# Performance work log

Hardware: AMD Instinct MI355X
Metric: run time of the kernel (lower is better)

The kernel has to match this reference:

```python
import jax, jax.numpy as jnp
import numpy as np

N_EMBD = 1024
N_HEAD = 16
B, T = 2, 2048


def setup_inputs() -> dict:
    key = jax.random.key(0)
    ks = jax.random.split(key, 9)
    s = 1.0 / np.sqrt(N_EMBD)
    return {
        "x": jax.random.normal(ks[0], (B, T, N_EMBD), dtype=jnp.float32),
        "Wq": jax.random.normal(ks[1], (N_EMBD, N_EMBD), dtype=jnp.float32) * s,
        "bq": jax.random.normal(ks[2], (N_EMBD,), dtype=jnp.float32) * s,
        "Wk": jax.random.normal(ks[3], (N_EMBD, N_EMBD), dtype=jnp.float32) * s,
        "bk": jax.random.normal(ks[4], (N_EMBD,), dtype=jnp.float32) * s,
        "Wv": jax.random.normal(ks[5], (N_EMBD, N_EMBD), dtype=jnp.float32) * s,
        "bv": jax.random.normal(ks[6], (N_EMBD,), dtype=jnp.float32) * s,
        "Wp": jax.random.normal(ks[7], (N_EMBD, N_EMBD), dtype=jnp.float32) * s,
        "bp": jax.random.normal(ks[8], (N_EMBD,), dtype=jnp.float32) * s,
    }


def reference(x, Wq, bq, Wk, bk, Wv, bv, Wp, bp):
    b, t, c = x.shape
    hd = c // N_HEAD  # head dim
    # torch Linear: x @ W.T + b; reshape to (B, H, T, hd)
    def heads(W, bias):
        return (x @ W.T + bias).reshape(b, t, N_HEAD, hd).transpose(0, 2, 1, 3)
    q, k, v = heads(Wq, bq), heads(Wk, bk), heads(Wv, bv)
    scale = 1.0 / np.sqrt(hd)
    att = jnp.einsum("bhqd,bhkd->bhqk", q, k) * scale  # (B,H,T,T)
    causal = jnp.tril(jnp.ones((t, t), dtype=bool))
    att = jnp.where(causal[None, None], att, -jnp.inf)
    att = jax.nn.softmax(att, axis=-1)
    y = jnp.einsum("bhqk,bhkd->bhqd", att, v)
    y = y.transpose(0, 2, 1, 3).reshape(b, t, c)
    return y @ Wp.T + bp
```

## Files before the change

### kernel.cpp

```cpp
#include <hip/hip_runtime.h>

typedef __bf16 bf16x8 __attribute__((ext_vector_type(8)));
typedef __bf16 bf16x4 __attribute__((ext_vector_type(4)));
typedef float f32x4 __attribute__((ext_vector_type(4)));

#define DEVI __device__ __forceinline__

constexpr int NE = 1024;
constexpr int NH = 16;
constexpr int HD = 64;
constexpr int BB = 2;
constexpr int TT = 2048;
constexpr int MM = BB * TT;

DEVI unsigned short f2bf(float f) {
  union { float f; unsigned u; } v; v.f = f;
  unsigned r = v.u + 0x7FFFu + ((v.u >> 16) & 1u);
  return (unsigned short)(r >> 16);
}

__global__ __launch_bounds__(256) void cvt_bf16(const float* __restrict__ in,
                                                unsigned short* __restrict__ out, int n4) {
  int i = blockIdx.x * blockDim.x + threadIdx.x;
  if (i >= n4) return;
  float4 v = reinterpret_cast<const float4*>(in)[i];
  ushort4 o;
  o.x = f2bf(v.x); o.y = f2bf(v.y); o.z = f2bf(v.z); o.w = f2bf(v.w);
  reinterpret_cast<ushort4*>(out)[i] = o;
}

__global__ __launch_bounds__(256) void cvt_w(const float* __restrict__ q, const float* __restrict__ k,
                                             const float* __restrict__ v, const float* __restrict__ p,
                                             unsigned short* __restrict__ out) {
  int i = blockIdx.x * blockDim.x + threadIdx.x;
  const int seg = i >> 18;
  const float* src = (seg == 0) ? q : (seg == 1) ? k : (seg == 2) ? v : p;
  float4 vv = reinterpret_cast<const float4*>(src)[i & 0x3FFFF];
  ushort4 o;
  o.x = f2bf(vv.x); o.y = f2bf(vv.y); o.z = f2bf(vv.z); o.w = f2bf(vv.w);
  reinterpret_cast<ushort4*>(out)[i] = o;
}

template <int BM, int MODE>
__global__ __launch_bounds__(256, (BM == 128) ? 3 : 2)
void gemm_nt(const unsigned short* __restrict__ A, const unsigned short* __restrict__ Bm,
             const float* __restrict__ b0, const float* __restrict__ b1, const float* __restrict__ b2,
             void* __restrict__ o0, unsigned short* __restrict__ o1, unsigned short* __restrict__ o2,
             int K, int nbx) {
  constexpr int WAVES_N = (BM == 128) ? 2 : 4;
  constexpr int NJ = (BM == 128) ? 4 : 2;
  constexpr int A_LPW = BM / 64;
  __shared__ __align__(16) unsigned short As[3][BM * 32];
  __shared__ __align__(16) unsigned short Bs[3][128 * 32];
  const int tid = threadIdx.x;
  const int wid = tid >> 6;
  const int lane = tid & 63;
  const int l15 = lane & 15, l4 = lane >> 4;

  const int id = blockIdx.x;
  const int chunk = gridDim.x >> 3;
  const int idp = (id & 7) * chunk + (id >> 3);
  const int bx = idp / (gridDim.x / nbx), by = idp % (gridDim.x / nbx);

  const int brow = by * BM;
  const int bcol = bx * 128;
  const int wm = wid / WAVES_N, wn = wid % WAVES_N;
  const int wmoff = wm * 64;
  const int wnoff = wn * (128 / WAVES_N);

  f32x4 acc[4][NJ] = {};

  const int srow = lane >> 2;
  const int sscol = ((lane & 3) ^ ((lane >> 3) & 3)) * 8;

  auto stage = [&](int buf, int t) {
    const int kb = t * 32;
#pragma unroll
    for (int c = 0; c < A_LPW; ++c) {
      const int rb = wid * (BM / 4) + c * 16;
      __builtin_amdgcn_global_load_lds(
          (const __attribute__((address_space(1))) void*)(A + (size_t)(brow + rb + srow) * K + kb + sscol),
          (__attribute__((address_space(3))) void*)&As[buf][rb * 32], 16, 0, 0);
    }
#pragma unroll
    for (int c = 0; c < 2; ++c) {
      const int rb = wid * 32 + c * 16;
      __builtin_amdgcn_global_load_lds(
          (const __attribute__((address_space(1))) void*)(Bm + (size_t)(bcol + rb + srow) * K + kb + sscol),
          (__attribute__((address_space(3))) void*)&Bs[buf][rb * 32], 16, 0, 0);
    }
  };

  const int roff = l15 * 32 + (l4 ^ ((l15 >> 1) & 3)) * 8;

  auto compute = [&](int cb) {
    bf16x8 af[4], bfj[NJ];
#pragma unroll
    for (int i = 0; i < 4; ++i)
      af[i] = *reinterpret_cast<const bf16x8*>(&As[cb][(wmoff + i * 16) * 32 + roff]);
#pragma unroll
    for (int j = 0; j < NJ; ++j)
      bfj[j] = *reinterpret_cast<const bf16x8*>(&Bs[cb][(wnoff + j * 16) * 32 + roff]);
#pragma unroll
    for (int i = 0; i < 4; ++i)
#pragma unroll
      for (int j = 0; j < NJ; ++j)
        acc[i][j] = __builtin_amdgcn_mfma_f32_16x16x32_bf16(af[i], bfj[j], acc[i][j], 0, 0, 0);
  };

  const int NT = K / 32;
  stage(0, 0);
  stage(1, 1);
  int cb = 0, sb = 2;
  for (int t = 0; t + 2 < NT; ++t) {
    stage(sb, t + 2);
    if constexpr (BM == 128) asm volatile("s_waitcnt vmcnt(8)" ::: "memory");
    else                     asm volatile("s_waitcnt vmcnt(6)" ::: "memory");
    asm volatile("s_barrier" ::: "memory");
    compute(cb);
    asm volatile("s_barrier" ::: "memory");
    sb = cb;
    cb = (cb == 2) ? 0 : cb + 1;
  }
  if constexpr (BM == 128) asm volatile("s_waitcnt vmcnt(4)" ::: "memory");
  else                     asm volatile("s_waitcnt vmcnt(3)" ::: "memory");
  asm volatile("s_barrier" ::: "memory");
  compute(cb);
  asm volatile("s_barrier" ::: "memory");
  cb = (cb == 2) ? 0 : cb + 1;
  asm volatile("s_waitcnt vmcnt(0)" ::: "memory");
  asm volatile("s_barrier" ::: "memory");
  compute(cb);

  if (MODE == 0) {
#pragma unroll
    for (int j = 0; j < NJ; ++j) {
      const int col = bcol + wnoff + j * 16 + l15;
      const float bv = b0[col];
#pragma unroll
      for (int i = 0; i < 4; ++i) {
        const int row0 = brow + wmoff + i * 16 + l4 * 4;
#pragma unroll
        for (int r = 0; r < 4; ++r)
          ((float*)o0)[(size_t)(row0 + r) * NE + col] = acc[i][j][r] + bv;
      }
    }
  } else {
    const int seg = bcol >> 10;
    const float* bsel = (seg == 0) ? b0 : (seg == 1) ? b1 : b2;
    unsigned short* qk = (seg == 0) ? (unsigned short*)o0 : o1;
#pragma unroll
    for (int j = 0; j < NJ; ++j) {
      const int col = bcol + wnoff + j * 16 + l15;
      const int dcol = col & 1023;
      const int h = dcol >> 6, d = dcol & 63;
      const float bv = bsel[dcol];
#pragma unroll
      for (int i = 0; i < 4; ++i) {
        const int row0 = brow + wmoff + i * 16 + l4 * 4;
#pragma unroll
        for (int r = 0; r < 4; ++r) {
          const int row = row0 + r;
          const int b = row >> 11, t = row & (TT - 1);
          const unsigned short val = f2bf(acc[i][j][r] + bv);
          if (seg < 2)
            qk[((size_t)((b * NH + h) * TT + t) << 6) + d] = val;
          else
            o2[((size_t)(b * NH + h) * HD + d) * TT + t] = val;
        }
      }
    }
  }
}

__global__ __launch_bounds__(256, 2)
void attn(const unsigned short* __restrict__ Q, const unsigned short* __restrict__ Kk,
          const unsigned short* __restrict__ Vt, unsigned short* __restrict__ Y) {
  __shared__ __align__(16) unsigned short Ks[2][128 * 64];
  __shared__ __align__(16) unsigned short Vs[2][64 * 128];
  __shared__ __align__(16) unsigned short Pw[4][32 * 64];
  const int tid = threadIdx.x, wid = tid >> 6, lane = tid & 63;
  const int l15 = lane & 15, l4 = lane >> 4;

  const int id = blockIdx.x;
  const int j = id & 255, kk = id >> 8;
  const int bh = (j & 15) + 16 * kk;
  const int xt = kk ? 15 - (j >> 4) : (j >> 4);

  const int qw = xt * 128 + wid * 32;
  const int nkb = xt + 1;
  const unsigned short* Qh = Q + (size_t)bh * TT * HD;
  const unsigned short* Kh = Kk + (size_t)bh * TT * HD;
  const unsigned short* Vh = Vt + (size_t)bh * HD * TT;

  bf16x8 qf[2][2];
#pragma unroll
  for (int qt = 0; qt < 2; ++qt)
#pragma unroll
    for (int ks = 0; ks < 2; ++ks) {
      bf16x8 t = *reinterpret_cast<const bf16x8*>(&Qh[(qw + qt * 16 + l15) * 64 + ks * 32 + l4 * 8]);
#pragma unroll
      for (int e = 0; e < 8; ++e) t[e] = (__bf16)((float)t[e] * 0.18033688011f);
      qf[qt][ks] = t;
    }

  float m_[2] = {-3e38f, -3e38f};
  float l_[2] = {0.f, 0.f};
  f32x4 accO[4][2] = {};

  auto stage = [&](int buf, int kb) {
#pragma unroll
    for (int c = 0; c < 4; ++c) {
      const int row = wid * 32 + c * 8 + (lane >> 3);
      const int sc = ((lane & 7) ^ (lane >> 3)) * 8;
      __builtin_amdgcn_global_load_lds(
          (const __attribute__((address_space(1))) void*)(Kh + (size_t)(kb + row) * 64 + sc),
          (__attribute__((address_space(3))) void*)&Ks[buf][(wid * 32 + c * 8) * 64], 16, 0, 0);
    }
#pragma unroll
    for (int c = 0; c < 4; ++c) {
      const int row = wid * 16 + c * 4 + (lane >> 4);
      const int sc = ((lane & 15) ^ (c * 4 + (lane >> 4))) * 8;
      __builtin_amdgcn_global_load_lds(
          (const __attribute__((address_space(1))) void*)(Vh + (size_t)row * TT + kb + sc),
          (__attribute__((address_space(3))) void*)&Vs[buf][(wid * 16 + c * 4) * 128], 16, 0, 0);
    }
  };

  stage(0, 0);
  int cur = 0;
  for (int kbi = 0; kbi < nkb; ++kbi) {
    const int kb = kbi * 128;
    __syncthreads();
    if (kbi + 1 < nkb) stage(cur ^ 1, kb + 128);

    const bool diag = (kbi == nkb - 1);
    const char* ksb = (const char*)Ks[cur];
    const char* vsb = (const char*)Vs[cur];
    char* pwb = (char*)&Pw[wid][0];

    f32x4 z[8][2];
    __builtin_amdgcn_s_setprio(1);
#pragma unroll
    for (int kt = 0; kt < 8; ++kt) {
      const int row = kt * 16 + l15;
      const char* base = ksb + row * 128;
      bf16x8 kf0 = *reinterpret_cast<const bf16x8*>(base + (((0 + l4) ^ (l15 & 7)) << 4));
      bf16x8 kf1 = *reinterpret_cast<const bf16x8*>(base + (((4 + l4) ^ (l15 & 7)) << 4));
#pragma unroll
      for (int qt = 0; qt < 2; ++qt) {
        f32x4 zz = {};
        zz = __builtin_amdgcn_mfma_f32_16x16x32_bf16(kf0, qf[qt][0], zz, 0, 0, 0);
        zz = __builtin_amdgcn_mfma_f32_16x16x32_bf16(kf1, qf[qt][1], zz, 0, 0, 0);
        z[kt][qt] = zz;
      }
    }
    __builtin_amdgcn_s_setprio(0);

    if (diag) {
#pragma unroll
      for (int kt = 0; kt < 8; ++kt)
#pragma unroll
        for (int qt = 0; qt < 2; ++qt)
#pragma unroll
          for (int r = 0; r < 4; ++r) {
            const int key = kb + kt * 16 + l4 * 4 + r;
            const int qi = qw + qt * 16 + l15;
            z[kt][qt][r] = (key <= qi) ? z[kt][qt][r] : -3e38f;
          }
    }

#pragma unroll
    for (int qt = 0; qt < 2; ++qt) {
      float tm[16];
#pragma unroll
      for (int i = 0; i < 16; ++i)
        tm[i] = fmaxf(z[(2 * i) >> 2][qt][(2 * i) & 3], z[(2 * i + 1) >> 2][qt][(2 * i + 1) & 3]);
#pragma unroll
      for (int i = 0; i < 8; ++i) tm[i] = fmaxf(tm[i], tm[i + 8]);
#pragma unroll
      for (int i = 0; i < 4; ++i) tm[i] = fmaxf(tm[i], tm[i + 4]);
      float pm = fmaxf(fmaxf(tm[0], tm[2]), fmaxf(tm[1], tm[3]));
      pm = fmaxf(pm, __shfl_xor(pm, 16, 64));
      pm = fmaxf(pm, __shfl_xor(pm, 32, 64));

      if (!__all(pm <= m_[qt] + 11.5f)) {
        const float mn = fmaxf(m_[qt], pm);
        const float sf = exp2f(m_[qt] - mn);
        m_[qt] = mn;
        l_[qt] *= sf;
#pragma unroll
        for (int dt = 0; dt < 4; ++dt)
#pragma unroll
          for (int r = 0; r < 4; ++r) accO[dt][qt][r] *= sf;
      }

#pragma unroll
      for (int kt = 0; kt < 8; ++kt)
#pragma unroll
        for (int r = 0; r < 4; ++r)
          z[kt][qt][r] = exp2f(z[kt][qt][r] - m_[qt]);
      float ts[16];
#pragma unroll
      for (int i = 0; i < 16; ++i)
        ts[i] = z[(2 * i) >> 2][qt][(2 * i) & 3] + z[(2 * i + 1) >> 2][qt][(2 * i + 1) & 3];
#pragma unroll
      for (int i = 0; i < 8; ++i) ts[i] += ts[i + 8];
#pragma unroll
      for (int i = 0; i < 4; ++i) ts[i] += ts[i + 4];
      float rs = (ts[0] + ts[2]) + (ts[1] + ts[3]);
      rs += __shfl_xor(rs, 16, 64);
      rs += __shfl_xor(rs, 32, 64);
      l_[qt] += rs;
    }

#pragma unroll
    for (int h = 0; h < 2; ++h) {
#pragma unroll
      for (int qt = 0; qt < 2; ++qt) {
        const int q = qt * 16 + l15;
#pragma unroll
        for (int k4 = 0; k4 < 4; ++k4) {
          const int kt = h * 4 + k4;
          bf16x4 pk;
#pragma unroll
          for (int r = 0; r < 4; ++r) pk[r] = (__bf16)z[kt][qt][r];
          const int c16 = k4 * 2 + (l4 >> 1);
          *reinterpret_cast<bf16x4*>(pwb + q * 128 + ((c16 ^ (q & 7)) << 4) + (l4 & 1) * 8) = pk;
        }
      }
      asm volatile("s_waitcnt lgkmcnt(0)" ::: "memory");
      __builtin_amdgcn_sched_barrier(0);

      __builtin_amdgcn_s_setprio(1);
#pragma unroll
      for (int ks2 = 0; ks2 < 2; ++ks2) {
        bf16x8 pb[2];
#pragma unroll
        for (int qt = 0; qt < 2; ++qt) {
          const int q = qt * 16 + l15;
          pb[qt] = *reinterpret_cast<const bf16x8*>(pwb + q * 128 + ((((ks2 << 2) + l4) ^ (q & 7)) << 4));
        }
#pragma unroll
        for (int dt = 0; dt < 4; ++dt) {
          const int row = dt * 16 + l15;
          bf16x8 vf = *reinterpret_cast<const bf16x8*>(
              vsb + row * 256 + ((((h * 2 + ks2) * 4 + l4) ^ l15) << 4));
#pragma unroll
          for (int qt = 0; qt < 2; ++qt)
            accO[dt][qt] = __builtin_amdgcn_mfma_f32_16x16x32_bf16(vf, pb[qt], accO[dt][qt], 0, 0, 0);
        }
      }
      __builtin_amdgcn_s_setprio(0);
      __builtin_amdgcn_sched_barrier(0);
    }
    cur ^= 1;
  }

  const int b = bh >> 4, h = bh & 15;
#pragma unroll
  for (int qt = 0; qt < 2; ++qt) {
    const float inv = 1.0f / l_[qt];
    const int q = qw + qt * 16 + l15;
#pragma unroll
    for (int dt = 0; dt < 4; ++dt) {
      bf16x4 o;
#pragma unroll
      for (int r = 0; r < 4; ++r) o[r] = (__bf16)(accO[dt][qt][r] * inv);
      *reinterpret_cast<bf16x4*>(&Y[((size_t)(b * TT + q)) * NE + h * 64 + dt * 16 + l4 * 4]) = o;
    }
  }
}

extern "C" void kernel_launch(void* const* d_in, const int* in_sizes, int n_in,
                              void* d_out, int out_size, void* d_ws, size_t ws_size,
                              hipStream_t stream) {
  const float* x  = (const float*)d_in[0];
  const float* Wq = (const float*)d_in[1];
  const float* bq = (const float*)d_in[2];
  const float* Wk = (const float*)d_in[3];
  const float* bk = (const float*)d_in[4];
  const float* Wv = (const float*)d_in[5];
  const float* bv = (const float*)d_in[6];
  const float* Wp = (const float*)d_in[7];
  const float* bp = (const float*)d_in[8];

  char* ws = (char*)d_ws;
  const size_t MB = 1u << 20;
  unsigned short* xb   = (unsigned short*)(ws + 0 * MB);
  unsigned short* Wqkv = (unsigned short*)(ws + 8 * MB);
  unsigned short* Wpb  = (unsigned short*)(ws + 14 * MB);
  unsigned short* Qb   = (unsigned short*)(ws + 16 * MB);
  unsigned short* Kb   = (unsigned short*)(ws + 24 * MB);
  unsigned short* Vtb  = (unsigned short*)(ws + 32 * MB);
  unsigned short* yb   = (unsigned short*)(ws + 40 * MB);

  cvt_bf16<<<MM * NE / 4 / 256, 256, 0, stream>>>(x, xb, MM * NE / 4);
  cvt_w<<<4 * NE * NE / 4 / 256, 256, 0, stream>>>(Wq, Wk, Wv, Wp, Wqkv);

  gemm_nt<128, 1><<<768, 256, 0, stream>>>(xb, Wqkv, bq, bk, bv, Qb, Kb, Vtb, NE, 24);

  attn<<<512, 256, 0, stream>>>(Qb, Kb, Vtb, yb);

  gemm_nt<64, 0><<<512, 256, 0, stream>>>(yb, Wpb, bp, nullptr, nullptr, d_out, nullptr, nullptr, NE, 8);
}
```

Measured before the change: 214.9 us.

## Split KV range for long causal query tiles and merge partials in combine kernel

The attention grid is remapped so query tiles 8-15 are each split into two KV-range chunks, giving 768 blocks of more uniform length instead of 512 blocks with up to 16 KV tiles each. Split blocks write unnormalized bf16 partial outputs plus running max and sum to workspace, reusing the buffers of the no-longer-needed bf16 x and QKV weights. A new combine kernel merges the two partials with log-sum-exp weights. This is meant to shorten the longest causal blocks. The cost is an extra launch, extra global traffic for the partials, and bf16 rounding of the unnormalized partial outputs.

```diff
diff --git a/kernel.cpp b/kernel.cpp
--- a/kernel.cpp
+++ b/kernel.cpp
@@ -175,7 +175,8 @@
 
 __global__ __launch_bounds__(256, 2)
 void attn(const unsigned short* __restrict__ Q, const unsigned short* __restrict__ Kk,
-          const unsigned short* __restrict__ Vt, unsigned short* __restrict__ Y) {
+          const unsigned short* __restrict__ Vt, unsigned short* __restrict__ Y,
+          unsigned short* __restrict__ pO, float* __restrict__ pML) {
   __shared__ __align__(16) unsigned short Ks[2][128 * 64];
   __shared__ __align__(16) unsigned short Vs[2][64 * 128];
   __shared__ __align__(16) unsigned short Pw[4][32 * 64];
@@ -183,12 +184,23 @@
   const int l15 = lane & 15, l4 = lane >> 4;
 
   const int id = blockIdx.x;
-  const int j = id & 255, kk = id >> 8;
-  const int bh = (j & 15) + 16 * kk;
-  const int xt = kk ? 15 - (j >> 4) : (j >> 4);
+  const int x8 = id & 7;
+  const int c = id >> 3;
+  const int g = c / 24;
+  const int j = c % 24;
+  const int bh = g * 8 + x8;
+  int xt, t0, t1, chunk;
+  bool split;
+  if (j < 8) {
+    xt = j; t0 = 0; t1 = xt + 1; split = false; chunk = 0;
+  } else {
+    const int j2 = j - 8;
+    xt = 8 + (j2 >> 1); chunk = j2 & 1;
+    const int n = xt + 1, half = (n + 1) >> 1;
+    t0 = chunk ? half : 0; t1 = chunk ? n : half; split = true;
+  }
 
   const int qw = xt * 128 + wid * 32;
-  const int nkb = xt + 1;
   const unsigned short* Qh = Q + (size_t)bh * TT * HD;
   const unsigned short* Kh = Kk + (size_t)bh * TT * HD;
   const unsigned short* Vh = Vt + (size_t)bh * HD * TT;
@@ -210,31 +222,31 @@
 
   auto stage = [&](int buf, int kb) {
 #pragma unroll
-    for (int c = 0; c < 4; ++c) {
-      const int row = wid * 32 + c * 8 + (lane >> 3);
+    for (int cc = 0; cc < 4; ++cc) {
+      const int row = wid * 32 + cc * 8 + (lane >> 3);
       const int sc = ((lane & 7) ^ (lane >> 3)) * 8;
       __builtin_amdgcn_global_load_lds(
           (const __attribute__((address_space(1))) void*)(Kh + (size_t)(kb + row) * 64 + sc),
-          (__attribute__((address_space(3))) void*)&Ks[buf][(wid * 32 + c * 8) * 64], 16, 0, 0);
-    }
-#pragma unroll
-    for (int c = 0; c < 4; ++c) {
-      const int row = wid * 16 + c * 4 + (lane >> 4);
-      const int sc = ((lane & 15) ^ (c * 4 + (lane >> 4))) * 8;
+          (__attribute__((address_space(3))) void*)&Ks[buf][(wid * 32 + cc * 8) * 64], 16, 0, 0);
+    }
+#pragma unroll
+    for (int cc = 0; cc < 4; ++cc) {
+      const int row = wid * 16 + cc * 4 + (lane >> 4);
+      const int sc = ((lane & 15) ^ (cc * 4 + (lane >> 4))) * 8;
       __builtin_amdgcn_global_load_lds(
           (const __attribute__((address_space(1))) void*)(Vh + (size_t)row * TT + kb + sc),
-          (__attribute__((address_space(3))) void*)&Vs[buf][(wid * 16 + c * 4) * 128], 16, 0, 0);
+          (__attribute__((address_space(3))) void*)&Vs[buf][(wid * 16 + cc * 4) * 128], 16, 0, 0);
     }
   };
 
-  stage(0, 0);
+  stage(0, t0 * 128);
   int cur = 0;
-  for (int kbi = 0; kbi < nkb; ++kbi) {
+  for (int kbi = t0; kbi < t1; ++kbi) {
     const int kb = kbi * 128;
     __syncthreads();
-    if (kbi + 1 < nkb) stage(cur ^ 1, kb + 128);
-
-    const bool diag = (kbi == nkb - 1);
+    if (kbi + 1 < t1) stage(cur ^ 1, kb + 128);
+
+    const bool diag = (kbi == xt);
     const char* ksb = (const char*)Ks[cur];
     const char* vsb = (const char*)Vs[cur];
     char* pwb = (char*)&Pw[wid][0];
@@ -357,18 +369,72 @@
     cur ^= 1;
   }
 
+  if (!split) {
+    const int b = bh >> 4, h = bh & 15;
+#pragma unroll
+    for (int qt = 0; qt < 2; ++qt) {
+      const float inv = 1.0f / l_[qt];
+      const int q = qw + qt * 16 + l15;
+#pragma unroll
+      for (int dt = 0; dt < 4; ++dt) {
+        bf16x4 o;
+#pragma unroll
+        for (int r = 0; r < 4; ++r) o[r] = (__bf16)(accO[dt][qt][r] * inv);
+        *reinterpret_cast<bf16x4*>(&Y[((size_t)(b * TT + q)) * NE + h * 64 + dt * 16 + l4 * 4]) = o;
+      }
+    }
+  } else {
+    const int slot = ((bh << 3) + (xt - 8)) * 2 + chunk;
+#pragma unroll
+    for (int qt = 0; qt < 2; ++qt) {
+      const int ql = wid * 32 + qt * 16 + l15;
+#pragma unroll
+      for (int dt = 0; dt < 4; ++dt) {
+        bf16x4 o;
+#pragma unroll
+        for (int r = 0; r < 4; ++r) o[r] = (__bf16)accO[dt][qt][r];
+        *reinterpret_cast<bf16x4*>(&pO[((size_t)slot * 128 + ql) * 64 + dt * 16 + l4 * 4]) = o;
+      }
+      if (l4 == 0) {
+        pML[((size_t)slot * 128 + ql) * 2 + 0] = m_[qt];
+        pML[((size_t)slot * 128 + ql) * 2 + 1] = l_[qt];
+      }
+    }
+  }
+}
+
+__global__ __launch_bounds__(256)
+void combine(const unsigned short* __restrict__ pO, const float* __restrict__ pML,
+             unsigned short* __restrict__ Y) {
+  const int id = blockIdx.x;
+  const int bh = id >> 3, xti = id & 7;
+  const int xt = 8 + xti;
+  const int tid = threadIdx.x;
+  const int q = tid >> 1, dh = (tid & 1) * 32;
+
+  const int slot0 = ((bh << 3) + xti) * 2;
+  const float m0 = pML[((size_t)slot0 * 128 + q) * 2 + 0];
+  const float l0 = pML[((size_t)slot0 * 128 + q) * 2 + 1];
+  const float m1 = pML[((size_t)(slot0 + 1) * 128 + q) * 2 + 0];
+  const float l1 = pML[((size_t)(slot0 + 1) * 128 + q) * 2 + 1];
+  const float M = fmaxf(m0, m1);
+  const float w0 = exp2f(m0 - M), w1 = exp2f(m1 - M);
+  const float inv = 1.0f / (w0 * l0 + w1 * l1);
+
+  const unsigned short* a0 = &pO[((size_t)slot0 * 128 + q) * 64 + dh];
+  const unsigned short* a1 = &pO[((size_t)(slot0 + 1) * 128 + q) * 64 + dh];
   const int b = bh >> 4, h = bh & 15;
-#pragma unroll
-  for (int qt = 0; qt < 2; ++qt) {
-    const float inv = 1.0f / l_[qt];
-    const int q = qw + qt * 16 + l15;
-#pragma unroll
-    for (int dt = 0; dt < 4; ++dt) {
-      bf16x4 o;
-#pragma unroll
-      for (int r = 0; r < 4; ++r) o[r] = (__bf16)(accO[dt][qt][r] * inv);
-      *reinterpret_cast<bf16x4*>(&Y[((size_t)(b * TT + q)) * NE + h * 64 + dt * 16 + l4 * 4]) = o;
-    }
+  const int qg = xt * 128 + q;
+  unsigned short* yo = &Y[((size_t)(b * TT + qg)) * NE + h * 64 + dh];
+#pragma unroll
+  for (int v = 0; v < 4; ++v) {
+    bf16x8 x0 = *reinterpret_cast<const bf16x8*>(a0 + v * 8);
+    bf16x8 x1 = *reinterpret_cast<const bf16x8*>(a1 + v * 8);
+    bf16x8 o;
+#pragma unroll
+    for (int e = 0; e < 8; ++e)
+      o[e] = (__bf16)((w0 * (float)x0[e] + w1 * (float)x1[e]) * inv);
+    *reinterpret_cast<bf16x8*>(yo + v * 8) = o;
   }
 }
 
@@ -394,13 +460,16 @@
   unsigned short* Kb   = (unsigned short*)(ws + 24 * MB);
   unsigned short* Vtb  = (unsigned short*)(ws + 32 * MB);
   unsigned short* yb   = (unsigned short*)(ws + 40 * MB);
+  unsigned short* pO   = (unsigned short*)(ws + 0 * MB);
+  float*          pML  = (float*)(ws + 8 * MB);
 
   cvt_bf16<<<MM * NE / 4 / 256, 256, 0, stream>>>(x, xb, MM * NE / 4);
   cvt_w<<<4 * NE * NE / 4 / 256, 256, 0, stream>>>(Wq, Wk, Wv, Wp, Wqkv);
 
   gemm_nt<128, 1><<<768, 256, 0, stream>>>(xb, Wqkv, bq, bk, bv, Qb, Kb, Vtb, NE, 24);
 
-  attn<<<512, 256, 0, stream>>>(Qb, Kb, Vtb, yb);
+  attn<<<768, 256, 0, stream>>>(Qb, Kb, Vtb, yb, pO, pML);
+  combine<<<256, 256, 0, stream>>>(pO, pML, yb);
 
   gemm_nt<64, 0><<<512, 256, 0, stream>>>(yb, Wpb, bp, nullptr, nullptr, d_out, nullptr, nullptr, NE, 8);
 }
```

Measured after the change: 226.6 us. 5.4% more time.
